# Kernel optimization log

Measured on AMD Instinct MI355X. Metric: run time of the kernel, lower is better.

Reference implementation:

```python
import jax, jax.numpy as jnp
import numpy as np

GAE_GAMMA = 0.99
GAE_LAMBDA = 0.95
T, N_ENVS = 4096, 2048


def setup_inputs() -> dict:
    key = jax.random.key(0)
    k1, k2, k3, k4 = jax.random.split(key, 4)
    rewards = jax.random.normal(k1, (T, N_ENVS), dtype=jnp.float32)
    values = jax.random.normal(k2, (T, N_ENVS), dtype=jnp.float32)
    next_values = jax.random.normal(k3, (T, N_ENVS), dtype=jnp.float32)
    next_dones = jax.random.randint(k4, (T, N_ENVS), 0, 2).astype(jnp.bool_)
    return {"rewards": rewards, "values": values,
            "next_values": next_values, "next_dones": next_dones}


def reference(rewards, values, next_values, next_dones):
    gamma = jnp.asarray(GAE_GAMMA, rewards.dtype)
    lam = jnp.asarray(GAE_LAMBDA, rewards.dtype)
    not_done = 1.0 - next_dones.astype(rewards.dtype)  # ~next_dones
    # deltas[t] = r[t] + gamma * V(s_{t+1}) * ~done[t] - V(s_t)
    deltas = rewards + gamma * next_values * not_done - values
    gae_discount = gamma * lam

    def step(running_gae, inp):
        delta_t, nd_t = inp
        g = delta_t + gae_discount * nd_t * running_gae
        return g, g

    init = jnp.zeros_like(rewards[0])
    # reverse-time scan over the recurrence
    _, adv = jax.lax.scan(step, init, (deltas, not_done), reverse=True)
    returns = adv + values
    return adv, returns
```

## Files before the change

kernel.cpp:

```cpp
#include <hip/hip_runtime.h>

#define TT    4096
#define NENV  2048
#define N4    (NENV / 4)
#define L     8
#define NCH   (TT / L)
#define NBLK  (NCH * 2)

#define GAMMA 0.99f
#define GL    (0.99f * 0.95f)

#define STEP_AB(r_, v_, nv_, dn_, A_, B_)                    \
    {                                                        \
        const float nd = (dn_) ? 0.0f : 1.0f;                \
        const float di = (r_) + GAMMA * (nv_) * nd - (v_);   \
        const float c  = GL * nd;                            \
        (B_) = di + c * (B_);                                \
        (A_) = c * (A_);                                     \
    }

#define STEP_OUT(r_, v_, nv_, dn_, g_, adv_, ret_)           \
    {                                                        \
        const float nd = (dn_) ? 0.0f : 1.0f;                \
        const float di = (r_) + GAMMA * (nv_) * nd - (v_);   \
        (g_) = di + GL * nd * (g_);                          \
        (adv_) = (g_);                                       \
        (ret_) = (g_) + (v_);                                \
    }

#define P2_PREFETCH(abuf, bbuf, grp_)                        \
    _Pragma("unroll")                                        \
    for (int j = 0; j < 16; ++j) {                           \
        const int c = NCH - 1 - (grp_) * 16 - j;             \
        abuf[j] = As[c * NENV + col];                        \
        bbuf[j] = Bs[c * NENV + col];                        \
    }

#define P2_PROCESS(abuf, bbuf, grp_)                         \
    _Pragma("unroll")                                        \
    for (int j = 0; j < 16; ++j) {                           \
        const int c = NCH - 1 - (grp_) * 16 - j;             \
        Bs[c * NENV + col] = g;      \
        g = fmaf(abuf[j], g, bbuf[j]);                       \
    }

__global__ __launch_bounds__(256, 4) void gae_k1(
    const float4* __restrict__ rp,  const float4* __restrict__ vp,
    const float4* __restrict__ np,  const int4*   __restrict__ dp,
    float4* __restrict__ wsA, float4* __restrict__ wsB)
{
    const int chunk = (int)blockIdx.x >> 1;
    const int c4    = (((int)blockIdx.x & 1) << 8) | (int)threadIdx.x;
    const int base  = chunk * (L * N4) + c4;

    float4 R[L], V[L], NV[L]; int4 DN[L];
#pragma unroll
    for (int i = 0; i < L; ++i) R[i]  = rp[base + i * N4];
#pragma unroll
    for (int i = 0; i < L; ++i) NV[i] = np[base + i * N4];
#pragma unroll
    for (int i = 0; i < L; ++i) V[i]  = vp[base + i * N4];
#pragma unroll
    for (int i = 0; i < L; ++i) DN[i] = dp[base + i * N4];

    float Ax = 1.f, Ay = 1.f, Az = 1.f, Aw = 1.f;
    float Bx = 0.f, By = 0.f, Bz = 0.f, Bw = 0.f;
#pragma unroll
    for (int i = L - 1; i >= 0; --i) {
        STEP_AB(R[i].x, V[i].x, NV[i].x, DN[i].x, Ax, Bx);
        STEP_AB(R[i].y, V[i].y, NV[i].y, DN[i].y, Ay, By);
        STEP_AB(R[i].z, V[i].z, NV[i].z, DN[i].z, Az, Bz);
        STEP_AB(R[i].w, V[i].w, NV[i].w, DN[i].w, Aw, Bw);
    }
    wsA[chunk * N4 + c4] = make_float4(Ax, Ay, Az, Aw);
    wsB[chunk * N4 + c4] = make_float4(Bx, By, Bz, Bw);
}

__global__ __launch_bounds__(64) void gae_k2(
    const float* __restrict__ As, float* __restrict__ Bs)
{
    const int col = (int)blockIdx.x * 64 + (int)threadIdx.x;
    float a0[16], b0[16], a1[16], b1[16];
    float g = 0.0f;
    P2_PREFETCH(a0, b0, 0)
    for (int grp = 0; grp < NCH / 16; grp += 2) {
        P2_PREFETCH(a1, b1, grp + 1)
        P2_PROCESS(a0, b0, grp)
        if (grp + 2 < NCH / 16) { P2_PREFETCH(a0, b0, grp + 2) }
        P2_PROCESS(a1, b1, grp + 1)
    }
}

__global__ __launch_bounds__(256, 4) void gae_k3(
    const float4* __restrict__ rp,  const float4* __restrict__ vp,
    const float4* __restrict__ np,  const int4*   __restrict__ dp,
    const float4* __restrict__ gin,
    float4* __restrict__ adv4, float4* __restrict__ ret4)
{
    const int chunk = (int)blockIdx.x >> 1;
    const int c4    = (((int)blockIdx.x & 1) << 8) | (int)threadIdx.x;
    const int base  = chunk * (L * N4) + c4;

    const float4 g0 = gin[chunk * N4 + c4];

    float4 R[L], V[L], NV[L]; int4 DN[L];
#pragma unroll
    for (int i = 0; i < L; ++i) R[i]  = rp[base + i * N4];
#pragma unroll
    for (int i = 0; i < L; ++i) NV[i] = np[base + i * N4];
#pragma unroll
    for (int i = 0; i < L; ++i) V[i]  = vp[base + i * N4];
#pragma unroll
    for (int i = 0; i < L; ++i) DN[i] = dp[base + i * N4];

    float gx = g0.x, gy = g0.y, gz = g0.z, gw = g0.w;
#pragma unroll
    for (int i = L - 1; i >= 0; --i) {
        float4 a, t;
        STEP_OUT(R[i].x, V[i].x, NV[i].x, DN[i].x, gx, a.x, t.x);
        STEP_OUT(R[i].y, V[i].y, NV[i].y, DN[i].y, gy, a.y, t.y);
        STEP_OUT(R[i].z, V[i].z, NV[i].z, DN[i].z, gz, a.z, t.z);
        STEP_OUT(R[i].w, V[i].w, NV[i].w, DN[i].w, gw, a.w, t.w);
        adv4[base + i * N4] = a;
        ret4[base + i * N4] = t;
    }
}

extern "C" void kernel_launch(void* const* d_in, const int* in_sizes, int n_in,
                              void* d_out, int out_size, void* d_ws, size_t ws_size,
                              hipStream_t stream) {
    const float4* rp = (const float4*)d_in[0];
    const float4* vp = (const float4*)d_in[1];
    const float4* np = (const float4*)d_in[2];
    const int4*   dp = (const int4*)d_in[3];

    float4* adv4 = (float4*)d_out;
    float4* ret4 = adv4 + (size_t)TT * N4;

    float4* wsA = (float4*)d_ws;
    float4* wsB = wsA + (size_t)NCH * N4;

    gae_k1<<<NBLK, 256, 0, stream>>>(rp, vp, np, dp, wsA, wsB);
    gae_k2<<<NENV / 64, 64, 0, stream>>>((const float*)wsA, (float*)wsB);
    gae_k3<<<NBLK, 256, 0, stream>>>(rp, vp, np, dp, wsB, adv4, ret4);
}
```

Before: 210.1 us.

## Narrow per-thread width to float2, double blocks, stream loads, nontemporal stores

Each thread now handles 2 columns instead of 4, so twice as many blocks are launched and the launch bound asks for 8 waves per SIMD. The upfront register arrays holding all L timesteps are replaced by per-step loads inside the loop, which cuts register pressure. Output stores in the third kernel use nontemporal hints so they do not pollute the cache. The trade-off is narrower 8-byte memory transactions and less explicit load batching, which could reduce memory-level parallelism per thread.

```diff
diff --git a/kernel.cpp b/kernel.cpp
--- a/kernel.cpp
+++ b/kernel.cpp
@@ -2,13 +2,16 @@
 
 #define TT    4096
 #define NENV  2048
-#define N4    (NENV / 4)
+#define N2    (NENV / 2)
 #define L     8
 #define NCH   (TT / L)
-#define NBLK  (NCH * 2)
+#define BPC   4
+#define NBLK  (NCH * BPC)
 
 #define GAMMA 0.99f
 #define GL    (0.99f * 0.95f)
+
+typedef float v2f __attribute__((ext_vector_type(2)));
 
 #define STEP_AB(r_, v_, nv_, dn_, A_, B_)                    \
     {                                                        \
@@ -44,36 +47,29 @@
         g = fmaf(abuf[j], g, bbuf[j]);                       \
     }
 
-__global__ __launch_bounds__(256, 4) void gae_k1(
-    const float4* __restrict__ rp,  const float4* __restrict__ vp,
-    const float4* __restrict__ np,  const int4*   __restrict__ dp,
-    float4* __restrict__ wsA, float4* __restrict__ wsB)
+__global__ __launch_bounds__(256, 8) void gae_k1(
+    const float2* __restrict__ rp,  const float2* __restrict__ vp,
+    const float2* __restrict__ np,  const int2*   __restrict__ dp,
+    float2* __restrict__ wsA, float2* __restrict__ wsB)
 {
-    const int chunk = (int)blockIdx.x >> 1;
-    const int c4    = (((int)blockIdx.x & 1) << 8) | (int)threadIdx.x;
-    const int base  = chunk * (L * N4) + c4;
+    const int chunk = (int)blockIdx.x >> 2;
+    const int c2    = (((int)blockIdx.x & 3) << 8) | (int)threadIdx.x;
+    const int base  = chunk * (L * N2) + c2;
 
-    float4 R[L], V[L], NV[L]; int4 DN[L];
-#pragma unroll
-    for (int i = 0; i < L; ++i) R[i]  = rp[base + i * N4];
-#pragma unroll
-    for (int i = 0; i < L; ++i) NV[i] = np[base + i * N4];
-#pragma unroll
-    for (int i = 0; i < L; ++i) V[i]  = vp[base + i * N4];
-#pragma unroll
-    for (int i = 0; i < L; ++i) DN[i] = dp[base + i * N4];
-
-    float Ax = 1.f, Ay = 1.f, Az = 1.f, Aw = 1.f;
-    float Bx = 0.f, By = 0.f, Bz = 0.f, Bw = 0.f;
+    float Ax = 1.f, Ay = 1.f;
+    float Bx = 0.f, By = 0.f;
 #pragma unroll
     for (int i = L - 1; i >= 0; --i) {
-        STEP_AB(R[i].x, V[i].x, NV[i].x, DN[i].x, Ax, Bx);
-        STEP_AB(R[i].y, V[i].y, NV[i].y, DN[i].y, Ay, By);
-        STEP_AB(R[i].z, V[i].z, NV[i].z, DN[i].z, Az, Bz);
-        STEP_AB(R[i].w, V[i].w, NV[i].w, DN[i].w, Aw, Bw);
+        const int idx   = base + i * N2;
+        const float2 r  = rp[idx];
+        const float2 v  = vp[idx];
+        const float2 nv = np[idx];
+        const int2   dn = dp[idx];
+        STEP_AB(r.x, v.x, nv.x, dn.x, Ax, Bx);
+        STEP_AB(r.y, v.y, nv.y, dn.y, Ay, By);
     }
-    wsA[chunk * N4 + c4] = make_float4(Ax, Ay, Az, Aw);
-    wsB[chunk * N4 + c4] = make_float4(Bx, By, Bz, Bw);
+    wsA[chunk * N2 + c2] = make_float2(Ax, Ay);
+    wsB[chunk * N2 + c2] = make_float2(Bx, By);
 }
 
 __global__ __launch_bounds__(64) void gae_k2(
@@ -91,56 +87,50 @@
     }
 }
 
-__global__ __launch_bounds__(256, 4) void gae_k3(
-    const float4* __restrict__ rp,  const float4* __restrict__ vp,
-    const float4* __restrict__ np,  const int4*   __restrict__ dp,
-    const float4* __restrict__ gin,
-    float4* __restrict__ adv4, float4* __restrict__ ret4)
+__global__ __launch_bounds__(256, 8) void gae_k3(
+    const float2* __restrict__ rp,  const float2* __restrict__ vp,
+    const float2* __restrict__ np,  const int2*   __restrict__ dp,
+    const float2* __restrict__ gin,
+    float2* __restrict__ adv2, float2* __restrict__ ret2)
 {
-    const int chunk = (int)blockIdx.x >> 1;
-    const int c4    = (((int)blockIdx.x & 1) << 8) | (int)threadIdx.x;
-    const int base  = chunk * (L * N4) + c4;
+    const int chunk = (int)blockIdx.x >> 2;
+    const int c2    = (((int)blockIdx.x & 3) << 8) | (int)threadIdx.x;
+    const int base  = chunk * (L * N2) + c2;
 
-    const float4 g0 = gin[chunk * N4 + c4];
-
-    float4 R[L], V[L], NV[L]; int4 DN[L];
-#pragma unroll
-    for (int i = 0; i < L; ++i) R[i]  = rp[base + i * N4];
-#pragma unroll
-    for (int i = 0; i < L; ++i) NV[i] = np[base + i * N4];
-#pragma unroll
-    for (int i = 0; i < L; ++i) V[i]  = vp[base + i * N4];
-#pragma unroll
-    for (int i = 0; i < L; ++i) DN[i] = dp[base + i * N4];
-
-    float gx = g0.x, gy = g0.y, gz = g0.z, gw = g0.w;
+    const float2 g0 = gin[chunk * N2 + c2];
+    float gx = g0.x, gy = g0.y;
 #pragma unroll
     for (int i = L - 1; i >= 0; --i) {
-        float4 a, t;
-        STEP_OUT(R[i].x, V[i].x, NV[i].x, DN[i].x, gx, a.x, t.x);
-        STEP_OUT(R[i].y, V[i].y, NV[i].y, DN[i].y, gy, a.y, t.y);
-        STEP_OUT(R[i].z, V[i].z, NV[i].z, DN[i].z, gz, a.z, t.z);
-        STEP_OUT(R[i].w, V[i].w, NV[i].w, DN[i].w, gw, a.w, t.w);
-        adv4[base + i * N4] = a;
-        ret4[base + i * N4] = t;
+        const int idx   = base + i * N2;
+        const float2 r  = rp[idx];
+        const float2 v  = vp[idx];
+        const float2 nv = np[idx];
+        const int2   dn = dp[idx];
+        float ax, ay, tx, ty;
+        STEP_OUT(r.x, v.x, nv.x, dn.x, gx, ax, tx);
+        STEP_OUT(r.y, v.y, nv.y, dn.y, gy, ay, ty);
+        v2f av; av.x = ax; av.y = ay;
+        v2f tv; tv.x = tx; tv.y = ty;
+        __builtin_nontemporal_store(av, (v2f*)&adv2[idx]);
+        __builtin_nontemporal_store(tv, (v2f*)&ret2[idx]);
     }
 }
 
 extern "C" void kernel_launch(void* const* d_in, const int* in_sizes, int n_in,
                               void* d_out, int out_size, void* d_ws, size_t ws_size,
                               hipStream_t stream) {
-    const float4* rp = (const float4*)d_in[0];
-    const float4* vp = (const float4*)d_in[1];
-    const float4* np = (const float4*)d_in[2];
-    const int4*   dp = (const int4*)d_in[3];
+    const float2* rp = (const float2*)d_in[0];
+    const float2* vp = (const float2*)d_in[1];
+    const float2* np = (const float2*)d_in[2];
+    const int2*   dp = (const int2*)d_in[3];
 
-    float4* adv4 = (float4*)d_out;
-    float4* ret4 = adv4 + (size_t)TT * N4;
+    float2* adv2 = (float2*)d_out;
+    float2* ret2 = adv2 + (size_t)TT * N2;
 
-    float4* wsA = (float4*)d_ws;
-    float4* wsB = wsA + (size_t)NCH * N4;
+    float2* wsA = (float2*)d_ws;
+    float2* wsB = wsA + (size_t)NCH * N2;
 
     gae_k1<<<NBLK, 256, 0, stream>>>(rp, vp, np, dp, wsA, wsB);
     gae_k2<<<NENV / 64, 64, 0, stream>>>((const float*)wsA, (float*)wsB);
-    gae_k3<<<NBLK, 256, 0, stream>>>(rp, vp, np, dp, wsB, adv4, ret4);
+    gae_k3<<<NBLK, 256, 0, stream>>>(rp, vp, np, dp, wsB, adv2, ret2);
 }
```

Measured after the change: 208.9 us. About the same (-0.6%).
